# Performance work log

Measured on AMD Instinct MI355X. Metric: run time of the kernel, lower is better.

## Reference

```python
import jax, jax.numpy as jnp
import numpy as np

IDENT_SIZE = 100000
E = 1024      # embedding_dim == lstm input size
H = 2048      # hidden_dim
R = 1024      # remainder_dim
RULES = 50000 # rules_size


def setup_inputs() -> dict:
    key = jax.random.key(0)
    ks = jax.random.split(key, 12)
    def w(k, shape, scale=0.02):
        return jax.random.normal(k, shape, dtype=jnp.float32) * scale
    return {
        "ident": jax.random.randint(ks[0], (1,), 0, IDENT_SIZE),
        "remainder": jax.random.normal(ks[1], (1, 1, R), dtype=jnp.float32),
        "h0": jax.random.normal(ks[2], (1, 1, H), dtype=jnp.float32),
        "c0": jax.random.normal(ks[3], (1, 1, H), dtype=jnp.float32),
        "emb": w(ks[4], (IDENT_SIZE, E)),
        "W_rin": w(ks[5], (R, E)),   # linear_remainder_in, stored [in, out]
        "b_rin": jnp.zeros((E,), jnp.float32),
        "W_ih": w(ks[6], (4 * H, E)),  # torch LSTM weight_ih_l0, gate order i,f,g,o
        "W_hh": w(ks[7], (4 * H, H)),  # torch LSTM weight_hh_l0
        "b_ih": jnp.zeros((4 * H,), jnp.float32),
        "b_hh": jnp.zeros((4 * H,), jnp.float32),
        "W_ro": w(ks[8], (H, R)),      # linear_remainder_out
        "b_ro": jnp.zeros((R,), jnp.float32),
        "W_out": w(ks[9], (H, RULES)),  # linear_out
        "b_out": jnp.zeros((RULES,), jnp.float32),
    }


def reference(ident, remainder, h0, c0, emb, W_rin, b_rin, W_ih, W_hh,
              b_ih, b_hh, W_ro, b_ro, W_out, b_out):
    # embeds = embedding(ident).view((1,-1))  -> [1, E]
    embeds = emb[ident].reshape(1, -1)
    # inputs = embeds + relu(linear_remainder_in(remainder)) -> broadcast [1,1,E]
    x = embeds + jax.nn.relu(remainder @ W_rin + b_rin)  # [1,1,E]
    # single-step LSTM (seq=1, batch=1), torch gate order i, f, g, o
    gates = x @ W_ih.T + b_ih + h0 @ W_hh.T + b_hh  # [1,1,4H]
    i, f, g, o = jnp.split(gates, 4, axis=-1)
    c = jax.nn.sigmoid(f) * c0 + jax.nn.sigmoid(i) * jnp.tanh(g)
    h = jax.nn.sigmoid(o) * jnp.tanh(c)  # lstm_out == h for seq=1
    remainder_out = jax.nn.relu(h @ W_ro + b_ro)             # [1,1,R]
    out = jax.nn.log_softmax(jax.nn.relu(h @ W_out + b_out), axis=2)  # [1,1,RULES]
    return (out, (h, c), remainder_out)
```

## Files before the change

### kernel.cpp

```cpp
#include <hip/hip_runtime.h>
#include <math.h>

#define E_DIM 1024
#define H_DIM 2048
#define R_DIM 1024
#define RULES 50000

#define OUT_H  50000
#define OUT_C  52048
#define OUT_RO 54096

#define WS_XP    0
#define WS_H     8192
#define WS_CNT   10240
#define WS_PL    10256
#define WS_PRO   1610256
#define WS_BSUM  1643024

typedef float f32x4 __attribute__((ext_vector_type(4)));

__device__ __forceinline__ f32x4 nt4(const float* p) {
    return __builtin_nontemporal_load((const f32x4*)p);
}

__device__ __forceinline__ float sigf(float x) { return 1.f / (1.f + expf(-x)); }

__global__ __launch_bounds__(256) void k_x_partial(const float* __restrict__ rem,
    const float* __restrict__ W_rin, float* __restrict__ xp,
    unsigned int* __restrict__ cnt)
{
    if (blockIdx.x == 0 && blockIdx.y == 0 && threadIdx.x == 0) *cnt = 0u;
    __shared__ float rs[128];
    int ec = blockIdx.x, rc = blockIdx.y;
    if (threadIdx.x < 128) rs[threadIdx.x] = rem[rc * 128 + threadIdx.x];
    __syncthreads();
    int e = ec * 256 + threadIdx.x;
    const float* base = W_rin + (size_t)rc * 128 * E_DIM + e;
    float acc = 0.f;
#pragma unroll 8
    for (int rr = 0; rr < 128; ++rr)
        acc = fmaf(rs[rr], base[(size_t)rr * E_DIM], acc);
    xp[rc * E_DIM + e] = acc;
}

__global__ __launch_bounds__(256) void k_lstm(const float* __restrict__ xp,
    const float* __restrict__ b_rin, const float* __restrict__ emb,
    const int* __restrict__ ident,
    const float* __restrict__ h0, const float* __restrict__ c0,
    const float* __restrict__ W_ih, const float* __restrict__ W_hh,
    const float* __restrict__ b_ih, const float* __restrict__ b_hh,
    float* __restrict__ d_out, float* __restrict__ ws_h)
{
    __shared__ float xs[E_DIM];
    long long row = (long long)ident[0] * E_DIM;
#pragma unroll
    for (int e = threadIdx.x; e < E_DIM; e += 256) {
        float s = 0.f;
#pragma unroll
        for (int rc = 0; rc < 8; ++rc) s += xp[rc * E_DIM + e];
        xs[e] = emb[row + e] + fmaxf(s + b_rin[e], 0.f);
    }
    __syncthreads();

    int k = blockIdx.x;
    int w = threadIdx.x >> 6, lane = threadIdx.x & 63;
    int j = w * H_DIM + k;
    const float* Wi = W_ih + (size_t)j * E_DIM;
    const float* Wh = W_hh + (size_t)j * H_DIM;
    const f32x4* x4 = (const f32x4*)xs;
    const f32x4* h4 = (const f32x4*)h0;
    float acc = 0.f;
#pragma unroll
    for (int s = 0; s < 4; ++s) {
        int idx = s * 64 + lane;
        f32x4 wv = nt4(Wi + idx * 4);
        f32x4 xv = x4[idx];
        acc += wv.x * xv.x + wv.y * xv.y + wv.z * xv.z + wv.w * xv.w;
    }
#pragma unroll
    for (int s = 0; s < 8; ++s) {
        int idx = s * 64 + lane;
        f32x4 wv = nt4(Wh + idx * 4);
        f32x4 hv = h4[idx];
        acc += wv.x * hv.x + wv.y * hv.y + wv.z * hv.z + wv.w * hv.w;
    }
#pragma unroll
    for (int off = 32; off > 0; off >>= 1) acc += __shfl_xor(acc, off);
    __shared__ float gl[4];
    if (lane == 0) gl[w] = acc + b_ih[j] + b_hh[j];
    __syncthreads();
    if (threadIdx.x == 0) {
        float gi = gl[0], gf = gl[1], gg = gl[2], go = gl[3];
        float c = sigf(gf) * c0[k] + sigf(gi) * tanhf(gg);
        float h = sigf(go) * tanhf(c);
        d_out[OUT_H + k] = h;
        d_out[OUT_C + k] = c;
        ws_h[k] = h;
    }
}

__global__ __launch_bounds__(256) void k_big(const float* __restrict__ h,
    const float* __restrict__ W_out, const float* __restrict__ W_ro,
    float* __restrict__ pl, float* __restrict__ pro)
{
    __shared__ float hs[64];
    int hc = blockIdx.y;
    if (threadIdx.x < 64) hs[threadIdx.x] = h[hc * 64 + threadIdx.x];
    __syncthreads();
    if (blockIdx.x < 49) {
        int j0 = blockIdx.x * 1024 + threadIdx.x * 4;
        if (j0 >= RULES) return;
        f32x4 acc = {0.f, 0.f, 0.f, 0.f};
        const float* base = W_out + (size_t)hc * 64 * RULES + j0;
#pragma unroll 16
        for (int hh = 0; hh < 64; ++hh) {
            float hv = hs[hh];
            f32x4 wv = nt4(base + (size_t)hh * RULES);
            acc.x = fmaf(hv, wv.x, acc.x);
            acc.y = fmaf(hv, wv.y, acc.y);
            acc.z = fmaf(hv, wv.z, acc.z);
            acc.w = fmaf(hv, wv.w, acc.w);
        }
        *(f32x4*)(pl + (size_t)hc * RULES + j0) = acc;
    } else {
        int j0 = threadIdx.x * 4;
        f32x4 acc = {0.f, 0.f, 0.f, 0.f};
        const float* base = W_ro + (size_t)hc * 64 * R_DIM + j0;
#pragma unroll 16
        for (int hh = 0; hh < 64; ++hh) {
            float hv = hs[hh];
            f32x4 wv = nt4(base + (size_t)hh * R_DIM);
            acc.x = fmaf(hv, wv.x, acc.x);
            acc.y = fmaf(hv, wv.y, acc.y);
            acc.z = fmaf(hv, wv.z, acc.z);
            acc.w = fmaf(hv, wv.w, acc.w);
        }
        *(f32x4*)(pro + (size_t)hc * R_DIM + j0) = acc;
    }
}

__global__ __launch_bounds__(256) void k_tail(const float* __restrict__ pl,
    const float* __restrict__ b_out, const float* __restrict__ pro,
    const float* __restrict__ b_ro, unsigned int* __restrict__ cnt,
    float* __restrict__ bsum, float* __restrict__ d_out)
{
    if (blockIdx.x == 49) {
        int j0 = threadIdx.x * 4;
        f32x4 s = {0.f, 0.f, 0.f, 0.f};
#pragma unroll
        for (int hc = 0; hc < 32; ++hc) {
            f32x4 p = *(const f32x4*)(pro + (size_t)hc * R_DIM + j0);
            s.x += p.x; s.y += p.y; s.z += p.z; s.w += p.w;
        }
        const f32x4 b = *(const f32x4*)(b_ro + j0);
        f32x4 o;
        o.x = fmaxf(s.x + b.x, 0.f);
        o.y = fmaxf(s.y + b.y, 0.f);
        o.z = fmaxf(s.z + b.z, 0.f);
        o.w = fmaxf(s.w + b.w, 0.f);
        *(f32x4*)(d_out + OUT_RO + j0) = o;
        return;
    }
    int j0 = blockIdx.x * 1024 + threadIdx.x * 4;
    bool valid = j0 < RULES;
    f32x4 l = {0.f, 0.f, 0.f, 0.f};
    float se = 0.f;
    if (valid) {
        f32x4 s = {0.f, 0.f, 0.f, 0.f};
#pragma unroll
        for (int hc = 0; hc < 32; ++hc) {
            f32x4 p = *(const f32x4*)(pl + (size_t)hc * RULES + j0);
            s.x += p.x; s.y += p.y; s.z += p.z; s.w += p.w;
        }
        const f32x4 b = *(const f32x4*)(b_out + j0);
        l.x = fmaxf(s.x + b.x, 0.f);
        l.y = fmaxf(s.y + b.y, 0.f);
        l.z = fmaxf(s.z + b.z, 0.f);
        l.w = fmaxf(s.w + b.w, 0.f);
        se = expf(l.x) + expf(l.y) + expf(l.z) + expf(l.w);
    }
    __shared__ float red[256];
    red[threadIdx.x] = se;
    __syncthreads();
    for (int off = 128; off > 0; off >>= 1) {
        if (threadIdx.x < off) red[threadIdx.x] += red[threadIdx.x + off];
        __syncthreads();
    }
    __shared__ float lse_s;
    if (threadIdx.x == 0) {
        bsum[blockIdx.x] = red[0];
        __threadfence();
        __hip_atomic_fetch_add(cnt, 1u, __ATOMIC_RELEASE, __HIP_MEMORY_SCOPE_AGENT);
        while (__hip_atomic_load(cnt, __ATOMIC_ACQUIRE, __HIP_MEMORY_SCOPE_AGENT) < 49u) {}
        float ssum = 0.f;
        for (int i = 0; i < 49; ++i) ssum += bsum[i];
        lse_s = logf(ssum);
    }
    __syncthreads();
    if (valid) {
        f32x4 o;
        o.x = l.x - lse_s; o.y = l.y - lse_s; o.z = l.z - lse_s; o.w = l.w - lse_s;
        *(f32x4*)(d_out + j0) = o;
    }
}

extern "C" void kernel_launch(void* const* d_in, const int* in_sizes, int n_in,
                              void* d_out, int out_size, void* d_ws, size_t ws_size,
                              hipStream_t stream)
{
    const int*   ident = (const int*)  d_in[0];
    const float* rem   = (const float*)d_in[1];
    const float* h0    = (const float*)d_in[2];
    const float* c0    = (const float*)d_in[3];
    const float* emb   = (const float*)d_in[4];
    const float* W_rin = (const float*)d_in[5];
    const float* b_rin = (const float*)d_in[6];
    const float* W_ih  = (const float*)d_in[7];
    const float* W_hh  = (const float*)d_in[8];
    const float* b_ih  = (const float*)d_in[9];
    const float* b_hh  = (const float*)d_in[10];
    const float* W_ro  = (const float*)d_in[11];
    const float* b_ro  = (const float*)d_in[12];
    const float* W_out = (const float*)d_in[13];
    const float* b_out = (const float*)d_in[14];
    float* out = (float*)d_out;
    float* ws  = (float*)d_ws;
    unsigned int* cnt = (unsigned int*)(ws + WS_CNT);

    k_x_partial<<<dim3(4, 8), 256, 0, stream>>>(rem, W_rin, ws + WS_XP, cnt);
    k_lstm<<<2048, 256, 0, stream>>>(ws + WS_XP, b_rin, emb, ident,
                                     h0, c0, W_ih, W_hh, b_ih, b_hh,
                                     out, ws + WS_H);
    k_big<<<dim3(50, 32), 256, 0, stream>>>(ws + WS_H, W_out, W_ro,
                                            ws + WS_PL, ws + WS_PRO);
    k_tail<<<50, 256, 0, stream>>>(ws + WS_PL, b_out, ws + WS_PRO, b_ro,
                                   cnt, ws + WS_BSUM, out);
}
```

Baseline: 110.9 us.

## Move W_hh matvec into pre-kernel alongside W_rin and widen W_out tiles

The h0·W_hh^T gate contribution does not depend on x, so it now runs in the first kernel alongside the W_rin partial products. This fills the GPU in a stage that previously launched only 32 blocks. The LSTM kernel then only streams W_ih and adds the precomputed hh gates. The W_out projection kernel is also reshaped to a 1D grid with 8 outputs per thread, giving fewer, wider blocks. This adds a workspace buffer for the hh gates and changes the load balance of the big matvec.

```diff
diff --git a/kernel.cpp b/kernel.cpp
--- a/kernel.cpp
+++ b/kernel.cpp
@@ -11,85 +11,93 @@
 #define OUT_RO 54096
 
 #define WS_XP    0
-#define WS_H     8192
-#define WS_CNT   10240
-#define WS_PL    10256
-#define WS_PRO   1610256
-#define WS_BSUM  1643024
+#define WS_GH    8192
+#define WS_H     16384
+#define WS_BSUM  18432
+#define WS_CNT   18496
+#define WS_PL    18512
+#define WS_PRO   1618512
 
 typedef float f32x4 __attribute__((ext_vector_type(4)));
 
 __device__ __forceinline__ f32x4 nt4(const float* p) {
     return __builtin_nontemporal_load((const f32x4*)p);
 }
-
 __device__ __forceinline__ float sigf(float x) { return 1.f / (1.f + expf(-x)); }
 
-__global__ __launch_bounds__(256) void k_x_partial(const float* __restrict__ rem,
-    const float* __restrict__ W_rin, float* __restrict__ xp,
+__global__ __launch_bounds__(256) void k_pre(const float* __restrict__ rem,
+    const float* __restrict__ W_rin, const float* __restrict__ h0,
+    const float* __restrict__ W_hh, const float* __restrict__ b_hh,
+    float* __restrict__ xp, float* __restrict__ ghh,
     unsigned int* __restrict__ cnt)
 {
-    if (blockIdx.x == 0 && blockIdx.y == 0 && threadIdx.x == 0) *cnt = 0u;
-    __shared__ float rs[128];
-    int ec = blockIdx.x, rc = blockIdx.y;
-    if (threadIdx.x < 128) rs[threadIdx.x] = rem[rc * 128 + threadIdx.x];
-    __syncthreads();
-    int e = ec * 256 + threadIdx.x;
-    const float* base = W_rin + (size_t)rc * 128 * E_DIM + e;
-    float acc = 0.f;
+    const int bid = blockIdx.x, tid = threadIdx.x;
+    if (bid == 0 && tid == 0) *cnt = 0u;
+    if (bid < 2048) {
+        int w = tid >> 6, lane = tid & 63;
+        int j = bid * 4 + w;
+        const float* Wh = W_hh + (size_t)j * H_DIM;
+        const f32x4* h4 = (const f32x4*)h0;
+        float acc = 0.f;
+#pragma unroll
+        for (int s = 0; s < 8; ++s) {
+            int idx = s * 64 + lane;
+            f32x4 wv = nt4(Wh + idx * 4), hv = h4[idx];
+            acc += wv.x * hv.x + wv.y * hv.y + wv.z * hv.z + wv.w * hv.w;
+        }
+#pragma unroll
+        for (int off = 32; off > 0; off >>= 1) acc += __shfl_xor(acc, off);
+        if (lane == 0) ghh[j] = acc + b_hh[j];
+    } else {
+        __shared__ float rs[128];
+        int b = bid - 2048;
+        int ec = b & 3, rc = b >> 2;
+        if (tid < 128) rs[tid] = rem[rc * 128 + tid];
+        __syncthreads();
+        int e = ec * 256 + tid;
+        const float* base = W_rin + (size_t)(rc * 128) * E_DIM + e;
+        float acc = 0.f;
 #pragma unroll 8
-    for (int rr = 0; rr < 128; ++rr)
-        acc = fmaf(rs[rr], base[(size_t)rr * E_DIM], acc);
-    xp[rc * E_DIM + e] = acc;
+        for (int rr = 0; rr < 128; ++rr)
+            acc = fmaf(rs[rr], __builtin_nontemporal_load(base + (size_t)rr * E_DIM), acc);
+        xp[rc * E_DIM + e] = acc;
+    }
 }
 
 __global__ __launch_bounds__(256) void k_lstm(const float* __restrict__ xp,
     const float* __restrict__ b_rin, const float* __restrict__ emb,
-    const int* __restrict__ ident,
-    const float* __restrict__ h0, const float* __restrict__ c0,
-    const float* __restrict__ W_ih, const float* __restrict__ W_hh,
-    const float* __restrict__ b_ih, const float* __restrict__ b_hh,
-    float* __restrict__ d_out, float* __restrict__ ws_h)
+    const int* __restrict__ ident, const float* __restrict__ c0,
+    const float* __restrict__ W_ih, const float* __restrict__ b_ih,
+    const float* __restrict__ ghh, float* __restrict__ d_out,
+    float* __restrict__ ws_h)
 {
     __shared__ float xs[E_DIM];
+    __shared__ float gl[4];
+    const int tid = threadIdx.x, k = blockIdx.x;
     long long row = (long long)ident[0] * E_DIM;
-#pragma unroll
-    for (int e = threadIdx.x; e < E_DIM; e += 256) {
+    for (int e = tid; e < E_DIM; e += 256) {
         float s = 0.f;
 #pragma unroll
         for (int rc = 0; rc < 8; ++rc) s += xp[rc * E_DIM + e];
         xs[e] = emb[row + e] + fmaxf(s + b_rin[e], 0.f);
     }
     __syncthreads();
-
-    int k = blockIdx.x;
-    int w = threadIdx.x >> 6, lane = threadIdx.x & 63;
+    int w = tid >> 6, lane = tid & 63;
     int j = w * H_DIM + k;
     const float* Wi = W_ih + (size_t)j * E_DIM;
-    const float* Wh = W_hh + (size_t)j * H_DIM;
     const f32x4* x4 = (const f32x4*)xs;
-    const f32x4* h4 = (const f32x4*)h0;
     float acc = 0.f;
 #pragma unroll
     for (int s = 0; s < 4; ++s) {
         int idx = s * 64 + lane;
-        f32x4 wv = nt4(Wi + idx * 4);
-        f32x4 xv = x4[idx];
+        f32x4 wv = nt4(Wi + idx * 4), xv = x4[idx];
         acc += wv.x * xv.x + wv.y * xv.y + wv.z * xv.z + wv.w * xv.w;
     }
 #pragma unroll
-    for (int s = 0; s < 8; ++s) {
-        int idx = s * 64 + lane;
-        f32x4 wv = nt4(Wh + idx * 4);
-        f32x4 hv = h4[idx];
-        acc += wv.x * hv.x + wv.y * hv.y + wv.z * hv.z + wv.w * hv.w;
-    }
-#pragma unroll
     for (int off = 32; off > 0; off >>= 1) acc += __shfl_xor(acc, off);
-    __shared__ float gl[4];
-    if (lane == 0) gl[w] = acc + b_ih[j] + b_hh[j];
-    __syncthreads();
-    if (threadIdx.x == 0) {
+    if (lane == 0) gl[w] = acc + b_ih[j] + ghh[j];
+    __syncthreads();
+    if (tid == 0) {
         float gi = gl[0], gf = gl[1], gg = gl[2], go = gl[3];
         float c = sigf(gf) * c0[k] + sigf(gi) * tanhf(gg);
         float h = sigf(go) * tanhf(c);
@@ -104,36 +112,38 @@
     float* __restrict__ pl, float* __restrict__ pro)
 {
     __shared__ float hs[64];
-    int hc = blockIdx.y;
-    if (threadIdx.x < 64) hs[threadIdx.x] = h[hc * 64 + threadIdx.x];
-    __syncthreads();
-    if (blockIdx.x < 49) {
-        int j0 = blockIdx.x * 1024 + threadIdx.x * 4;
-        if (j0 >= RULES) return;
+    const int bid = blockIdx.x, tid = threadIdx.x;
+    int hc = (bid < 800) ? (bid / 25) : (bid - 800);
+    if (tid < 64) hs[tid] = h[hc * 64 + tid];
+    __syncthreads();
+    if (bid < 800) {
+        int j0 = (bid % 25) * 2048 + tid * 8;
+        if (j0 < RULES) {
+            f32x4 a0 = {0.f, 0.f, 0.f, 0.f}, a1 = {0.f, 0.f, 0.f, 0.f};
+            const float* base = W_out + (size_t)(hc * 64) * RULES + j0;
+#pragma unroll 8
+            for (int hh = 0; hh < 64; ++hh) {
+                float hv = hs[hh];
+                f32x4 w0 = nt4(base + (size_t)hh * RULES);
+                f32x4 w1 = nt4(base + (size_t)hh * RULES + 4);
+                a0.x = fmaf(hv, w0.x, a0.x); a0.y = fmaf(hv, w0.y, a0.y);
+                a0.z = fmaf(hv, w0.z, a0.z); a0.w = fmaf(hv, w0.w, a0.w);
+                a1.x = fmaf(hv, w1.x, a1.x); a1.y = fmaf(hv, w1.y, a1.y);
+                a1.z = fmaf(hv, w1.z, a1.z); a1.w = fmaf(hv, w1.w, a1.w);
+            }
+            *(f32x4*)(pl + (size_t)hc * RULES + j0) = a0;
+            *(f32x4*)(pl + (size_t)hc * RULES + j0 + 4) = a1;
+        }
+    } else {
+        int j0 = tid * 4;
         f32x4 acc = {0.f, 0.f, 0.f, 0.f};
-        const float* base = W_out + (size_t)hc * 64 * RULES + j0;
-#pragma unroll 16
-        for (int hh = 0; hh < 64; ++hh) {
-            float hv = hs[hh];
-            f32x4 wv = nt4(base + (size_t)hh * RULES);
-            acc.x = fmaf(hv, wv.x, acc.x);
-            acc.y = fmaf(hv, wv.y, acc.y);
-            acc.z = fmaf(hv, wv.z, acc.z);
-            acc.w = fmaf(hv, wv.w, acc.w);
-        }
-        *(f32x4*)(pl + (size_t)hc * RULES + j0) = acc;
-    } else {
-        int j0 = threadIdx.x * 4;
-        f32x4 acc = {0.f, 0.f, 0.f, 0.f};
-        const float* base = W_ro + (size_t)hc * 64 * R_DIM + j0;
+        const float* base = W_ro + (size_t)(hc * 64) * R_DIM + j0;
 #pragma unroll 16
         for (int hh = 0; hh < 64; ++hh) {
             float hv = hs[hh];
             f32x4 wv = nt4(base + (size_t)hh * R_DIM);
-            acc.x = fmaf(hv, wv.x, acc.x);
-            acc.y = fmaf(hv, wv.y, acc.y);
-            acc.z = fmaf(hv, wv.z, acc.z);
-            acc.w = fmaf(hv, wv.w, acc.w);
+            acc.x = fmaf(hv, wv.x, acc.x); acc.y = fmaf(hv, wv.y, acc.y);
+            acc.z = fmaf(hv, wv.z, acc.z); acc.w = fmaf(hv, wv.w, acc.w);
         }
         *(f32x4*)(pro + (size_t)hc * R_DIM + j0) = acc;
     }
@@ -198,8 +208,7 @@
     }
     __syncthreads();
     if (valid) {
-        f32x4 o;
-        o.x = l.x - lse_s; o.y = l.y - lse_s; o.z = l.z - lse_s; o.w = l.w - lse_s;
+        f32x4 o = {l.x - lse_s, l.y - lse_s, l.z - lse_s, l.w - lse_s};
         *(f32x4*)(d_out + j0) = o;
     }
 }
@@ -227,12 +236,12 @@
     float* ws  = (float*)d_ws;
     unsigned int* cnt = (unsigned int*)(ws + WS_CNT);
 
-    k_x_partial<<<dim3(4, 8), 256, 0, stream>>>(rem, W_rin, ws + WS_XP, cnt);
-    k_lstm<<<2048, 256, 0, stream>>>(ws + WS_XP, b_rin, emb, ident,
-                                     h0, c0, W_ih, W_hh, b_ih, b_hh,
-                                     out, ws + WS_H);
-    k_big<<<dim3(50, 32), 256, 0, stream>>>(ws + WS_H, W_out, W_ro,
-                                            ws + WS_PL, ws + WS_PRO);
+    k_pre<<<2080, 256, 0, stream>>>(rem, W_rin, h0, W_hh, b_hh,
+                                    ws + WS_XP, ws + WS_GH, cnt);
+    k_lstm<<<2048, 256, 0, stream>>>(ws + WS_XP, b_rin, emb, ident, c0,
+                                     W_ih, b_ih, ws + WS_GH, out, ws + WS_H);
+    k_big<<<832, 256, 0, stream>>>(ws + WS_H, W_out, W_ro,
+                                   ws + WS_PL, ws + WS_PRO);
     k_tail<<<50, 256, 0, stream>>>(ws + WS_PL, b_out, ws + WS_PRO, b_ro,
                                    cnt, ws + WS_BSUM, out);
 }
```

Result: slower. 132.3 us (+19.2%).
